# Optimization experiments

Hardware: AMD Instinct MI355X
Metric: run time of the kernel (lower is better)

## Reference

```python
import jax, jax.numpy as jnp
import numpy as np

B, T, V, H = 16, 256, 64, 256  # batch, time, num_inputs, hidden_dim
EPS = 1e-5

def _layernorm(h, g, b):
    mu = jnp.mean(h, axis=-1, keepdims=True)
    var = jnp.mean(jnp.square(h - mu), axis=-1, keepdims=True)
    return (h - mu) * jax.lax.rsqrt(var + EPS) * g + b

def setup_inputs() -> dict:
    key = jax.random.key(0)
    ks = jax.random.split(key, 16)
    s1, sH = 1.0, 1.0 / np.sqrt(H)
    sV = 1.0 / np.sqrt(V)
    inp = {
        "x": jax.random.normal(ks[0], (B, T, V), jnp.float32),
        # per-variable GRN params (input_dim=1), stacked over V
        "W1": jax.random.normal(ks[1], (V, H), jnp.float32) * s1,
        "b1": jnp.zeros((V, H), jnp.float32),
        "W2": jax.random.normal(ks[2], (V, H, H), jnp.float32) * sH,
        "b2": jnp.zeros((V, H), jnp.float32),
        "Wg": jax.random.normal(ks[3], (V, H), jnp.float32) * s1,  # first H rows of gate Linear(1,2H)
        "bg": jnp.zeros((V, H), jnp.float32),
        "Ws": jax.random.normal(ks[4], (V, H), jnp.float32) * s1,  # skip_proj Linear(1,H)
        "bs": jnp.zeros((V, H), jnp.float32),
        "g1": jnp.ones((V, H), jnp.float32),
        "be1": jnp.zeros((V, H), jnp.float32),
        # weight network GRN: V -> V, skip is Identity
        "nW1": jax.random.normal(ks[5], (V, V), jnp.float32) * sV,
        "nb1": jnp.zeros((V,), jnp.float32),
        "nW2": jax.random.normal(ks[6], (V, V), jnp.float32) * sV,
        "nb2": jnp.zeros((V,), jnp.float32),
        "nWg": jax.random.normal(ks[7], (V, V), jnp.float32) * sV,  # first V cols of gate Linear(V,2V)
        "nbg": jnp.zeros((V,), jnp.float32),
        "ng": jnp.ones((V,), jnp.float32),
        "nbe": jnp.zeros((V,), jnp.float32),
    }
    return inp

def reference(x, W1, b1, W2, b2, Wg, bg, Ws, bs, g1, be1,
              nW1, nb1, nW2, nb2, nWg, nbg, ng, nbe):
    # --- per-variable GRNs, vectorized over V (input is a scalar per variable) ---
    feat = x[..., None]                                     # [B,T,V,1]
    h1 = feat * W1 + b1                                     # [B,T,V,H]  fc1(1->H)
    res = jnp.einsum('btvh,vhk->btvk', jax.nn.elu(h1), W2) + b2  # fc2(H->H)
    gate = jax.nn.sigmoid(feat * Wg + bg)                   # gate(1->2H)[:H]
    skip = feat * Ws + bs                                   # skip_proj(1->H)
    var_out = _layernorm(skip + gate * res, g1, be1)        # [B,T,V,H]
    # --- weight network GRN on flattened input (V -> V, skip=Identity) ---
    wres = jnp.einsum('btv,vk->btk', jax.nn.elu(x @ nW1 + nb1), nW2) + nb2
    wgate = jax.nn.sigmoid(x @ nWg + nbg)
    wout = _layernorm(x + wgate * wres, ng, nbe)            # [B,T,V]
    weights = jax.nn.softmax(wout, axis=-1)                 # [B,T,V]
    combined = jnp.einsum('btvh,btv->bth', var_out, weights)  # [B,T,H]
    return combined
```

## Files before the change

### kernel.cpp

```cpp
#include <hip/hip_runtime.h>
#include <hip/hip_bf16.h>
#include <stdint.h>

#define NTOK 4096
#define NV 64
#define NH 256
#define LN_EPS 1e-5f

typedef __attribute__((ext_vector_type(8))) short short8;
typedef __attribute__((ext_vector_type(4))) float f32x4;
typedef __attribute__((ext_vector_type(4))) uint32_t u32x4;

__device__ __forceinline__ unsigned short f32_to_bf16(float f) {
    uint32_t u = __builtin_bit_cast(uint32_t, f);
    return (unsigned short)((u + 0x7FFFu + ((u >> 16) & 1u)) >> 16);
}
__device__ __forceinline__ float fsigmoid(float z) { return 1.0f / (1.0f + __expf(-z)); }
__device__ __forceinline__ float felu(float z) { return z > 0.0f ? z : (__expf(z) - 1.0f); }
__device__ __forceinline__ uint32_t pack_bf16x2(float ze, float zo) {
    const uint32_t ue = __builtin_bit_cast(uint32_t, ze) + 0x8000u;
    const uint32_t uo = __builtin_bit_cast(uint32_t, zo) + 0x8000u;
    return __builtin_amdgcn_perm(uo, ue, 0x07060302u);
}
__device__ __forceinline__ void gload16(const void* g, void* l) {
    __builtin_amdgcn_global_load_lds(
        (const __attribute__((address_space(1))) uint32_t*)g,
        (__attribute__((address_space(3))) uint32_t*)l, 16, 0, 0);
}

__global__ __launch_bounds__(256) void k_w2t(const float* __restrict__ W2,
                                             unsigned short* __restrict__ W2T) {
    __shared__ float tile[32][33];
    const int v  = blockIdx.x >> 6;
    const int t  = blockIdx.x & 63;
    const int h0 = (t & 7) * 32;
    const int o0 = (t >> 3) * 32;
    const int r  = threadIdx.x >> 3;
    const int c4 = (threadIdx.x & 7) * 4;
    const float4 d = *(const float4*)(W2 + ((size_t)v * NH + h0 + r) * NH + o0 + c4);
    tile[r][c4 + 0] = d.x; tile[r][c4 + 1] = d.y;
    tile[r][c4 + 2] = d.z; tile[r][c4 + 3] = d.w;
    __syncthreads();
    ushort4 o;
    o.x = f32_to_bf16(tile[c4 + 0][r]);
    o.y = f32_to_bf16(tile[c4 + 1][r]);
    o.z = f32_to_bf16(tile[c4 + 2][r]);
    o.w = f32_to_bf16(tile[c4 + 3][r]);
    *(ushort4*)(W2T + ((size_t)v * NH + o0 + r) * NH + h0 + c4) = o;
}

__global__ __launch_bounds__(256) void k_weights(
    const float* __restrict__ x,
    const float* __restrict__ nW1, const float* __restrict__ nb1,
    const float* __restrict__ nW2, const float* __restrict__ nb2,
    const float* __restrict__ nWg, const float* __restrict__ nbg,
    const float* __restrict__ ng,  const float* __restrict__ nbe,
    float* __restrict__ wout_buf) {
    const int wv = threadIdx.x >> 6;
    const int lane = threadIdx.x & 63;
    const int tok = blockIdx.x * 4 + wv;
    const float xv = x[(size_t)tok * NV + lane];
    float acc1 = nb1[lane], accg = nbg[lane];
#pragma unroll 8
    for (int k = 0; k < 64; ++k) {
        const float xk = __shfl(xv, k);
        acc1 = fmaf(xk, nW1[k * 64 + lane], acc1);
        accg = fmaf(xk, nWg[k * 64 + lane], accg);
    }
    const float h  = felu(acc1);
    const float wg = fsigmoid(accg);
    float acc2 = nb2[lane];
#pragma unroll 8
    for (int k = 0; k < 64; ++k) {
        const float hk = __shfl(h, k);
        acc2 = fmaf(hk, nW2[k * 64 + lane], acc2);
    }
    const float pre = xv + wg * acc2;
    float s = pre;
#pragma unroll
    for (int m = 32; m >= 1; m >>= 1) s += __shfl_xor(s, m);
    const float mu = s * (1.0f / 64.0f);
    const float dd = pre - mu;
    float s2 = dd * dd;
#pragma unroll
    for (int m = 32; m >= 1; m >>= 1) s2 += __shfl_xor(s2, m);
    const float inv = rsqrtf(s2 * (1.0f / 64.0f) + LN_EPS);
    const float wln = dd * inv * ng[lane] + nbe[lane];
    float mx = wln;
#pragma unroll
    for (int m = 32; m >= 1; m >>= 1) mx = fmaxf(mx, __shfl_xor(mx, m));
    const float e = __expf(wln - mx);
    float se = e;
#pragma unroll
    for (int m = 32; m >= 1; m >>= 1) se += __shfl_xor(se, m);
    wout_buf[(size_t)tok * NV + lane] = e / se;
}

__device__ __forceinline__ const float* row_ptr(int r, const float* W1, const float* b1,
                                                const float* Wg, const float* bg,
                                                const float* Ws, const float* bs,
                                                const float* b2, const float* g1,
                                                const float* be1) {
    switch (r) {
        case 0: return W1; case 1: return b1; case 2: return Wg; case 3: return bg;
        case 4: return Ws; case 5: return bs; case 6: return b2; case 7: return g1;
        default: return be1;
    }
}

__global__ __launch_bounds__(256, 2) void k_main(
    const float* __restrict__ x, const unsigned short* __restrict__ W2T,
    const float* __restrict__ W1, const float* __restrict__ b1,
    const float* __restrict__ Wg, const float* __restrict__ bg,
    const float* __restrict__ Ws, const float* __restrict__ bs,
    const float* __restrict__ b2, const float* __restrict__ g1,
    const float* __restrict__ be1, const float* __restrict__ wgts,
    float* __restrict__ partials,
    float* __restrict__ outacc) {
    __shared__ u32x4 sB[3][1024];
    __shared__ float sRB[2][9][256];
    __shared__ float sX[64][9];
    __shared__ float sW[64][9];

    const int tid  = threadIdx.x;
    const int wid  = tid >> 6, lane = tid & 63;
    const int c    = lane & 15, kg = lane >> 4;
    const int bid  = blockIdx.x;
    const int vg   = bid & 7, tt = bid >> 3;
    const int t0   = tt * 64, vbase = vg * 8;

    const float* r0p = row_ptr(2 * wid,     W1, b1, Wg, bg, Ws, bs, b2, g1, be1);
    const float* r1p = row_ptr(2 * wid + 1, W1, b1, Wg, bg, Ws, bs, b2, g1, be1);

    int bsrc[4], bdst[4];
#pragma unroll
    for (int q = 0; q < 4; ++q) {
        const int idx = wid * 256 + q * 64 + lane;
        const int o = idx >> 2, sl = idx & 3;
        const int s = (sl - (o >> 1)) & 3;
        bsrc[q] = o * NH + s * 8;
        bdst[q] = idx * 16;
    }

#define STAGE_B(vt, kt, buf)                                                     \
    do {                                                                         \
        const unsigned short* Wsrc_ = W2T + (size_t)(vt) * (NH * NH) + (kt) * 32;\
        char* dst_ = (char*)sB[buf];                                             \
        gload16(Wsrc_ + bsrc[0], dst_ + bdst[0]);                                \
        gload16(Wsrc_ + bsrc[1], dst_ + bdst[1]);                                \
        gload16(Wsrc_ + bsrc[2], dst_ + bdst[2]);                                \
        gload16(Wsrc_ + bsrc[3], dst_ + bdst[3]);                                \
    } while (0)

#define STAGE_ROWS(vt, rbuf)                                                     \
    do {                                                                         \
        gload16(r0p + (size_t)(vt) * NH + lane * 4,                              \
                (char*)sRB[rbuf] + (2 * wid) * 1024);                            \
        gload16(r1p + (size_t)(vt) * NH + lane * 4,                              \
                (char*)sRB[rbuf] + (2 * wid + 1) * 1024);                        \
        if (wid == 0)                                                            \
            gload16(be1 + (size_t)(vt) * NH + lane * 4,                          \
                    (char*)sRB[rbuf] + 8 * 1024);                                \
    } while (0)

    STAGE_B(vbase, 0, 0);
    STAGE_B(vbase, 1, 1);
    STAGE_ROWS(vbase, 0);
#pragma unroll
    for (int e = 0; e < 2; ++e) {
        const int ee = tid + e * 256;
        const int row = ee >> 3, cc = ee & 7;
        sX[row][cc] = x[(size_t)(t0 + row) * NV + vbase + cc];
        sW[row][cc] = wgts[(size_t)(t0 + row) * NV + vbase + cc];
    }
    __syncthreads();

    const int rdbase = c * 64 + (((kg + (c >> 1)) & 3) << 4);
    const f32x4 fzero = {0.f, 0.f, 0.f, 0.f};

    f32x4 wacc[16];
#pragma unroll
    for (int f = 0; f < 16; ++f) wacc[f] = fzero;

    int cur = 0;

#pragma unroll 1
    for (int vi = 0; vi < 8; ++vi) {
        const int rcur = vi & 1;
        const float xv = sX[wid * 16 + c][vi];

        f32x4 acc[16];
#pragma unroll
        for (int f = 0; f < 16; ++f) acc[f] = fzero;

#pragma unroll 1
        for (int ks = 0; ks < 8; ++ks) {
            asm volatile("s_waitcnt vmcnt(4)" ::: "memory");
            __builtin_amdgcn_sched_barrier(0);
            __builtin_amdgcn_s_barrier();

            const int k0 = ks * 32 + kg * 8;
            const float4 wA = *(const float4*)&sRB[rcur][0][k0];
            const float4 wB = *(const float4*)&sRB[rcur][0][k0 + 4];
            const float4 bA = *(const float4*)&sRB[rcur][1][k0];
            const float4 bB = *(const float4*)&sRB[rcur][1][k0 + 4];
            u32x4 ap;
            {
                const float z0 = fmaf(xv, wA.x, bA.x), z1 = fmaf(xv, wA.y, bA.y);
                const float z2 = fmaf(xv, wA.z, bA.z), z3 = fmaf(xv, wA.w, bA.w);
                const float z4 = fmaf(xv, wB.x, bB.x), z5 = fmaf(xv, wB.y, bB.y);
                const float z6 = fmaf(xv, wB.z, bB.z), z7 = fmaf(xv, wB.w, bB.w);
                ap[0] = pack_bf16x2(felu(z0), felu(z1));
                ap[1] = pack_bf16x2(felu(z2), felu(z3));
                ap[2] = pack_bf16x2(felu(z4), felu(z5));
                ap[3] = pack_bf16x2(felu(z6), felu(z7));
            }

            {
                const int nxt2 = (cur == 0) ? 2 : cur - 1;
                if (ks < 6) {
                    STAGE_B(vbase + vi, ks + 2, nxt2);
                } else if (vi < 7) {
                    STAGE_B(vbase + vi + 1, ks - 6, nxt2);
                    if (ks == 6) STAGE_ROWS(vbase + vi + 1, rcur ^ 1);
                }
            }

            const short8 af = __builtin_bit_cast(short8, ap);
            const char* bb = (const char*)sB[cur] + rdbase;
            __builtin_amdgcn_s_setprio(1);
#pragma unroll
            for (int f = 0; f < 16; ++f) {
                const short8 bf = __builtin_bit_cast(short8, *(const u32x4*)(bb + (f << 10)));
                acc[f] = __builtin_amdgcn_mfma_f32_16x16x32_bf16(af, bf, acc[f], 0, 0, 0);
            }
            __builtin_amdgcn_s_setprio(0);
            cur = (cur == 2) ? 0 : cur + 1;
        }

        float xr[4], wv_[4];
#pragma unroll
        for (int r = 0; r < 4; ++r) {
            const int tl = wid * 16 + kg * 4 + r;
            xr[r]  = sX[tl][vi];
            wv_[r] = sW[tl][vi];
        }
        float ps[4] = {}, pq[4] = {};
        float gv[16], bev[16];
#pragma unroll
        for (int f = 0; f < 16; ++f) {
            const int h = f * 16 + c;
            const float Wg_ = sRB[rcur][2][h], bg_ = sRB[rcur][3][h];
            const float Ws_ = sRB[rcur][4][h], bs_ = sRB[rcur][5][h];
            const float b2_ = sRB[rcur][6][h];
            gv[f] = sRB[rcur][7][h]; bev[f] = sRB[rcur][8][h];
#pragma unroll
            for (int r = 0; r < 4; ++r) {
                const float y = fmaf(xr[r], Ws_, bs_) +
                                fsigmoid(fmaf(xr[r], Wg_, bg_)) * (acc[f][r] + b2_);
                acc[f][r] = y;
                ps[r] += y;
                pq[r] = fmaf(y, y, pq[r]);
            }
        }
#pragma unroll
        for (int m = 1; m <= 8; m <<= 1)
#pragma unroll
            for (int r = 0; r < 4; ++r) {
                ps[r] += __shfl_xor(ps[r], m);
                pq[r] += __shfl_xor(pq[r], m);
            }
#pragma unroll
        for (int r = 0; r < 4; ++r) {
            const float mu = ps[r] * (1.0f / 256.0f);
            const float vr = fmaf(-mu, mu, pq[r] * (1.0f / 256.0f));
            const float iv = rsqrtf(vr + LN_EPS);
            const float wiv = wv_[r] * iv;
#pragma unroll
            for (int f = 0; f < 16; ++f)
                wacc[f][r] = fmaf(wiv * (acc[f][r] - mu), gv[f],
                                  fmaf(wv_[r], bev[f], wacc[f][r]));
        }
    }
#undef STAGE_B
#undef STAGE_ROWS

    const int tokb = t0 + wid * 16 + kg * 4;
    if (partials) {
        float* P = partials + (size_t)vg * NTOK * NH;
#pragma unroll
        for (int r = 0; r < 4; ++r) {
            float* rowp = P + (size_t)(tokb + r) * NH + c;
#pragma unroll
            for (int f = 0; f < 16; ++f) rowp[f * 16] = wacc[f][r];
        }
    } else {
#pragma unroll
        for (int r = 0; r < 4; ++r) {
            float* rowp = outacc + (size_t)(tokb + r) * NH + c;
#pragma unroll
            for (int f = 0; f < 16; ++f) atomicAdd(&rowp[f * 16], wacc[f][r]);
        }
    }
}

__global__ __launch_bounds__(256) void k_reduce(const float* __restrict__ P,
                                                float* __restrict__ out) {
    const size_t i = ((size_t)blockIdx.x * 256 + threadIdx.x);
    const f32x4* P4 = (const f32x4*)P;
    f32x4 s = P4[i];
#pragma unroll
    for (int sl = 1; sl < 8; ++sl) s += P4[(size_t)sl * (NTOK * NH / 4) + i];
    ((f32x4*)out)[i] = s;
}

extern "C" void kernel_launch(void* const* d_in, const int* in_sizes, int n_in,
                              void* d_out, int out_size, void* d_ws, size_t ws_size,
                              hipStream_t stream) {
    const float* x   = (const float*)d_in[0];
    const float* W1  = (const float*)d_in[1];
    const float* b1  = (const float*)d_in[2];
    const float* W2  = (const float*)d_in[3];
    const float* b2  = (const float*)d_in[4];
    const float* Wg  = (const float*)d_in[5];
    const float* bg  = (const float*)d_in[6];
    const float* Ws  = (const float*)d_in[7];
    const float* bs  = (const float*)d_in[8];
    const float* g1  = (const float*)d_in[9];
    const float* be1 = (const float*)d_in[10];
    const float* nW1 = (const float*)d_in[11];
    const float* nb1 = (const float*)d_in[12];
    const float* nW2 = (const float*)d_in[13];
    const float* nb2 = (const float*)d_in[14];
    const float* nWg = (const float*)d_in[15];
    const float* nbg = (const float*)d_in[16];
    const float* ng  = (const float*)d_in[17];
    const float* nbe = (const float*)d_in[18];
    float* out = (float*)d_out;

    char* ws = (char*)d_ws;
    float* ws_wgt = (float*)ws;
    unsigned short* ws_W2T = (unsigned short*)(ws + (1 << 20));
    const size_t part_off = (size_t)9 << 20;
    const size_t part_bytes = (size_t)8 * NTOK * NH * 4;
    const bool use_part = ws_size >= part_off + part_bytes;
    float* ws_part = use_part ? (float*)(ws + part_off) : nullptr;

    k_w2t<<<dim3(64 * 64), dim3(256), 0, stream>>>(W2, ws_W2T);
    k_weights<<<dim3(NTOK / 4), dim3(256), 0, stream>>>(x, nW1, nb1, nW2, nb2,
                                                        nWg, nbg, ng, nbe, ws_wgt);
    if (!use_part) hipMemsetAsync(d_out, 0, (size_t)out_size * 4, stream);
    k_main<<<dim3(512), dim3(256), 0, stream>>>(x, ws_W2T, W1, b1, Wg, bg, Ws, bs,
                                                b2, g1, be1, ws_wgt, ws_part, out);
    if (use_part)
        k_reduce<<<dim3(NTOK * NH / 4 / 256), dim3(256), 0, stream>>>(ws_part, out);
}
```

Before: 141.3 us.

## Use packed FP32 math, hardware bf16 convert, and prescaled sigmoid via exp2

Rewrites the elementwise epilogue and the ELU/bf16 packing in the main kernel to use v_pk_fma/add/mul_f32 on pairs of values and v_cvt_pk_bf16_f32 for conversion. The gate weights and biases are pre-multiplied by -log2(e) in a new small kernel, so the sigmoid becomes exp2 plus a hardware reciprocal. The aim is to cut VALU instruction count in the per-token LayerNorm and gate math. The cost is an extra launch, a workspace offset shift, and slightly different rounding: round-to-nearest-even instead of the old round-half-up, plus the approximate rcp.

Measured after the change: 128.8 us. 1.1x faster.

```diff
diff --git a/kernel.cpp b/kernel.cpp
--- a/kernel.cpp
+++ b/kernel.cpp
@@ -9,18 +9,37 @@
 
 typedef __attribute__((ext_vector_type(8))) short short8;
 typedef __attribute__((ext_vector_type(4))) float f32x4;
+typedef __attribute__((ext_vector_type(2))) float f32x2;
 typedef __attribute__((ext_vector_type(4))) uint32_t u32x4;
 
+__device__ __forceinline__ f32x2 mk2(float a, float b) {
+    f32x2 r; r.x = a; r.y = b; return r;
+}
 __device__ __forceinline__ unsigned short f32_to_bf16(float f) {
     uint32_t u = __builtin_bit_cast(uint32_t, f);
     return (unsigned short)((u + 0x7FFFu + ((u >> 16) & 1u)) >> 16);
 }
 __device__ __forceinline__ float fsigmoid(float z) { return 1.0f / (1.0f + __expf(-z)); }
 __device__ __forceinline__ float felu(float z) { return z > 0.0f ? z : (__expf(z) - 1.0f); }
-__device__ __forceinline__ uint32_t pack_bf16x2(float ze, float zo) {
-    const uint32_t ue = __builtin_bit_cast(uint32_t, ze) + 0x8000u;
-    const uint32_t uo = __builtin_bit_cast(uint32_t, zo) + 0x8000u;
-    return __builtin_amdgcn_perm(uo, ue, 0x07060302u);
+__device__ __forceinline__ f32x2 pk_fma(f32x2 a, f32x2 b, f32x2 c) {
+    f32x2 d;
+    asm("v_pk_fma_f32 %0, %1, %2, %3" : "=v"(d) : "v"(a), "v"(b), "v"(c));
+    return d;
+}
+__device__ __forceinline__ f32x2 pk_add(f32x2 a, f32x2 b) {
+    f32x2 d;
+    asm("v_pk_add_f32 %0, %1, %2" : "=v"(d) : "v"(a), "v"(b));
+    return d;
+}
+__device__ __forceinline__ f32x2 pk_mul(f32x2 a, f32x2 b) {
+    f32x2 d;
+    asm("v_pk_mul_f32 %0, %1, %2" : "=v"(d) : "v"(a), "v"(b));
+    return d;
+}
+__device__ __forceinline__ uint32_t cvtpk_bf16(float lo, float hi) {
+    uint32_t r;
+    asm("v_cvt_pk_bf16_f32 %0, %1, %2" : "=v"(r) : "v"(lo), "v"(hi));
+    return r;
 }
 __device__ __forceinline__ void gload16(const void* g, void* l) {
     __builtin_amdgcn_global_load_lds(
@@ -49,6 +68,18 @@
     *(ushort4*)(W2T + ((size_t)v * NH + o0 + r) * NH + h0 + c4) = o;
 }
 
+__global__ __launch_bounds__(256) void k_scale(const float* __restrict__ Wg,
+                                               const float* __restrict__ bg,
+                                               float* __restrict__ Wg2,
+                                               float* __restrict__ bg2) {
+    const int i = blockIdx.x * 256 + threadIdx.x;
+    const float c = -1.44269504f;
+    const float4 a = ((const float4*)Wg)[i];
+    const float4 b = ((const float4*)bg)[i];
+    ((float4*)Wg2)[i] = float4{a.x * c, a.y * c, a.z * c, a.w * c};
+    ((float4*)bg2)[i] = float4{b.x * c, b.y * c, b.z * c, b.w * c};
+}
+
 __global__ __launch_bounds__(256) void k_weights(
     const float* __restrict__ x,
     const float* __restrict__ nW1, const float* __restrict__ nb1,
@@ -111,7 +142,7 @@
 __global__ __launch_bounds__(256, 2) void k_main(
     const float* __restrict__ x, const unsigned short* __restrict__ W2T,
     const float* __restrict__ W1, const float* __restrict__ b1,
-    const float* __restrict__ Wg, const float* __restrict__ bg,
+    const float* __restrict__ Wg2, const float* __restrict__ bg2,
     const float* __restrict__ Ws, const float* __restrict__ bs,
     const float* __restrict__ b2, const float* __restrict__ g1,
     const float* __restrict__ be1, const float* __restrict__ wgts,
@@ -129,8 +160,8 @@
     const int vg   = bid & 7, tt = bid >> 3;
     const int t0   = tt * 64, vbase = vg * 8;
 
-    const float* r0p = row_ptr(2 * wid,     W1, b1, Wg, bg, Ws, bs, b2, g1, be1);
-    const float* r1p = row_ptr(2 * wid + 1, W1, b1, Wg, bg, Ws, bs, b2, g1, be1);
+    const float* r0p = row_ptr(2 * wid,     W1, b1, Wg2, bg2, Ws, bs, b2, g1, be1);
+    const float* r1p = row_ptr(2 * wid + 1, W1, b1, Wg2, bg2, Ws, bs, b2, g1, be1);
 
     int bsrc[4], bdst[4];
 #pragma unroll
@@ -177,6 +208,7 @@
 
     const int rdbase = c * 64 + (((kg + (c >> 1)) & 3) << 4);
     const f32x4 fzero = {0.f, 0.f, 0.f, 0.f};
+    const f32x2 one2 = {1.0f, 1.0f};
 
     f32x4 wacc[16];
 #pragma unroll
@@ -188,6 +220,7 @@
     for (int vi = 0; vi < 8; ++vi) {
         const int rcur = vi & 1;
         const float xv = sX[wid * 16 + c][vi];
+        const f32x2 xv2 = {xv, xv};
 
         f32x4 acc[16];
 #pragma unroll
@@ -206,14 +239,14 @@
             const float4 bB = *(const float4*)&sRB[rcur][1][k0 + 4];
             u32x4 ap;
             {
-                const float z0 = fmaf(xv, wA.x, bA.x), z1 = fmaf(xv, wA.y, bA.y);
-                const float z2 = fmaf(xv, wA.z, bA.z), z3 = fmaf(xv, wA.w, bA.w);
-                const float z4 = fmaf(xv, wB.x, bB.x), z5 = fmaf(xv, wB.y, bB.y);
-                const float z6 = fmaf(xv, wB.z, bB.z), z7 = fmaf(xv, wB.w, bB.w);
-                ap[0] = pack_bf16x2(felu(z0), felu(z1));
-                ap[1] = pack_bf16x2(felu(z2), felu(z3));
-                ap[2] = pack_bf16x2(felu(z4), felu(z5));
-                ap[3] = pack_bf16x2(felu(z6), felu(z7));
+                const f32x2 z0 = pk_fma(xv2, mk2(wA.x, wA.y), mk2(bA.x, bA.y));
+                const f32x2 z1 = pk_fma(xv2, mk2(wA.z, wA.w), mk2(bA.z, bA.w));
+                const f32x2 z2 = pk_fma(xv2, mk2(wB.x, wB.y), mk2(bB.x, bB.y));
+                const f32x2 z3 = pk_fma(xv2, mk2(wB.z, wB.w), mk2(bB.z, bB.w));
+                ap[0] = cvtpk_bf16(felu(z0.x), felu(z0.y));
+                ap[1] = cvtpk_bf16(felu(z1.x), felu(z1.y));
+                ap[2] = cvtpk_bf16(felu(z2.x), felu(z2.y));
+                ap[3] = cvtpk_bf16(felu(z3.x), felu(z3.y));
             }
 
             {
@@ -245,24 +278,42 @@
             xr[r]  = sX[tl][vi];
             wv_[r] = sW[tl][vi];
         }
-        float ps[4] = {}, pq[4] = {};
-        float gv[16], bev[16];
+        const f32x2 xr01 = {xr[0], xr[1]}, xr23 = {xr[2], xr[3]};
+        f32x2 ps01 = {0.f, 0.f}, ps23 = {0.f, 0.f};
+        f32x2 pq01 = {0.f, 0.f}, pq23 = {0.f, 0.f};
 #pragma unroll
         for (int f = 0; f < 16; ++f) {
             const int h = f * 16 + c;
             const float Wg_ = sRB[rcur][2][h], bg_ = sRB[rcur][3][h];
             const float Ws_ = sRB[rcur][4][h], bs_ = sRB[rcur][5][h];
             const float b2_ = sRB[rcur][6][h];
-            gv[f] = sRB[rcur][7][h]; bev[f] = sRB[rcur][8][h];
-#pragma unroll
-            for (int r = 0; r < 4; ++r) {
-                const float y = fmaf(xr[r], Ws_, bs_) +
-                                fsigmoid(fmaf(xr[r], Wg_, bg_)) * (acc[f][r] + b2_);
-                acc[f][r] = y;
-                ps[r] += y;
-                pq[r] = fmaf(y, y, pq[r]);
-            }
-        }
+            const f32x2 Wgp = {Wg_, Wg_}, bgp = {bg_, bg_};
+            const f32x2 Wsp = {Ws_, Ws_}, bsp = {bs_, bs_}, b2p = {b2_, b2_};
+            const f32x2 a01 = {acc[f][0], acc[f][1]};
+            const f32x2 a23 = {acc[f][2], acc[f][3]};
+            const f32x2 zg01 = pk_fma(xr01, Wgp, bgp);
+            const f32x2 zg23 = pk_fma(xr23, Wgp, bgp);
+            const f32x2 e01 = {exp2f(zg01.x), exp2f(zg01.y)};
+            const f32x2 e23 = {exp2f(zg23.x), exp2f(zg23.y)};
+            const f32x2 d01 = pk_add(e01, one2);
+            const f32x2 d23 = pk_add(e23, one2);
+            const f32x2 s01 = {__builtin_amdgcn_rcpf(d01.x), __builtin_amdgcn_rcpf(d01.y)};
+            const f32x2 s23 = {__builtin_amdgcn_rcpf(d23.x), __builtin_amdgcn_rcpf(d23.y)};
+            const f32x2 R01 = pk_add(a01, b2p);
+            const f32x2 R23 = pk_add(a23, b2p);
+            const f32x2 sk01 = pk_fma(xr01, Wsp, bsp);
+            const f32x2 sk23 = pk_fma(xr23, Wsp, bsp);
+            const f32x2 y01 = pk_fma(s01, R01, sk01);
+            const f32x2 y23 = pk_fma(s23, R23, sk23);
+            ps01 = pk_add(ps01, y01);
+            ps23 = pk_add(ps23, y23);
+            pq01 = pk_fma(y01, y01, pq01);
+            pq23 = pk_fma(y23, y23, pq23);
+            acc[f][0] = y01.x; acc[f][1] = y01.y;
+            acc[f][2] = y23.x; acc[f][3] = y23.y;
+        }
+        float ps[4] = {ps01.x, ps01.y, ps23.x, ps23.y};
+        float pq[4] = {pq01.x, pq01.y, pq23.x, pq23.y};
 #pragma unroll
         for (int m = 1; m <= 8; m <<= 1)
 #pragma unroll
@@ -270,16 +321,32 @@
                 ps[r] += __shfl_xor(ps[r], m);
                 pq[r] += __shfl_xor(pq[r], m);
             }
+        float nmu[4], wiv[4];
 #pragma unroll
         for (int r = 0; r < 4; ++r) {
             const float mu = ps[r] * (1.0f / 256.0f);
             const float vr = fmaf(-mu, mu, pq[r] * (1.0f / 256.0f));
-            const float iv = rsqrtf(vr + LN_EPS);
-            const float wiv = wv_[r] * iv;
-#pragma unroll
-            for (int f = 0; f < 16; ++f)
-                wacc[f][r] = fmaf(wiv * (acc[f][r] - mu), gv[f],
-                                  fmaf(wv_[r], bev[f], wacc[f][r]));
+            nmu[r] = -mu;
+            wiv[r] = wv_[r] * rsqrtf(vr + LN_EPS);
+        }
+        const f32x2 nmu01 = {nmu[0], nmu[1]}, nmu23 = {nmu[2], nmu[3]};
+        const f32x2 wiv01 = {wiv[0], wiv[1]}, wiv23 = {wiv[2], wiv[3]};
+        const f32x2 wv01 = {wv_[0], wv_[1]}, wv23 = {wv_[2], wv_[3]};
+#pragma unroll
+        for (int f = 0; f < 16; ++f) {
+            const int h = f * 16 + c;
+            const float gv_ = sRB[rcur][7][h], bev_ = sRB[rcur][8][h];
+            const f32x2 gvp = {gv_, gv_}, bevp = {bev_, bev_};
+            f32x2 w01 = {wacc[f][0], wacc[f][1]};
+            f32x2 w23 = {wacc[f][2], wacc[f][3]};
+            const f32x2 y01 = {acc[f][0], acc[f][1]};
+            const f32x2 y23 = {acc[f][2], acc[f][3]};
+            const f32x2 t01 = pk_mul(pk_add(y01, nmu01), wiv01);
+            const f32x2 t23 = pk_mul(pk_add(y23, nmu23), wiv23);
+            w01 = pk_fma(t01, gvp, pk_fma(wv01, bevp, w01));
+            w23 = pk_fma(t23, gvp, pk_fma(wv23, bevp, w23));
+            wacc[f][0] = w01.x; wacc[f][1] = w01.y;
+            wacc[f][2] = w23.x; wacc[f][3] = w23.y;
         }
     }
 #undef STAGE_B
@@ -341,17 +408,21 @@
     char* ws = (char*)d_ws;
     float* ws_wgt = (float*)ws;
     unsigned short* ws_W2T = (unsigned short*)(ws + (1 << 20));
-    const size_t part_off = (size_t)9 << 20;
+    float* ws_Wg2 = (float*)(ws + (9 << 20));
+    float* ws_bg2 = (float*)(ws + (9 << 20) + (64 << 10));
+    const size_t part_off = (size_t)10 << 20;
     const size_t part_bytes = (size_t)8 * NTOK * NH * 4;
     const bool use_part = ws_size >= part_off + part_bytes;
     float* ws_part = use_part ? (float*)(ws + part_off) : nullptr;
 
     k_w2t<<<dim3(64 * 64), dim3(256), 0, stream>>>(W2, ws_W2T);
+    k_scale<<<dim3(16), dim3(256), 0, stream>>>(Wg, bg, ws_Wg2, ws_bg2);
     k_weights<<<dim3(NTOK / 4), dim3(256), 0, stream>>>(x, nW1, nb1, nW2, nb2,
                                                         nWg, nbg, ng, nbe, ws_wgt);
     if (!use_part) hipMemsetAsync(d_out, 0, (size_t)out_size * 4, stream);
-    k_main<<<dim3(512), dim3(256), 0, stream>>>(x, ws_W2T, W1, b1, Wg, bg, Ws, bs,
-                                                b2, g1, be1, ws_wgt, ws_part, out);
+    k_main<<<dim3(512), dim3(256), 0, stream>>>(x, ws_W2T, W1, b1, ws_Wg2, ws_bg2,
+                                                Ws, bs, b2, g1, be1, ws_wgt,
+                                                ws_part, out);
     if (use_part)
         k_reduce<<<dim3(NTOK * NH / 4 / 256), dim3(256), 0, stream>>>(ws_part, out);
 }
```
